# Performance work log

Measured on AMD Instinct MI355X. Metric: run time of the kernel, lower is better.

## Reference

```python
import jax, jax.numpy as jnp
import numpy as np

N_HEAD = 32
N_KV = 8
D = 2048
HD = D // N_HEAD
FF = 8192
EPS = 1e-5
THETA = 10000.0


def rms_norm(x, g):
    return g * x / jnp.sqrt(jnp.mean(x * x, axis=-1, keepdims=True) + EPS)


def rope(x):
    # x: [B, H, T, hd]; lucidrains interleaved RoPE
    T = x.shape[2]
    inv_freq = 1.0 / (THETA ** (jnp.arange(0, HD, 2, dtype=jnp.float32) / HD))  # [hd/2]
    freqs = jnp.arange(T, dtype=jnp.float32)[:, None] * inv_freq[None, :]       # [T, hd/2]
    freqs = jnp.repeat(freqs, 2, axis=-1)                                        # [T, hd]
    cos, sin = jnp.cos(freqs), jnp.sin(freqs)
    x1 = x[..., ::2]
    x2 = x[..., 1::2]
    rot = jnp.stack([-x2, x1], axis=-1).reshape(x.shape)
    return x * cos + rot * sin


def attention(x, wq, wk, wv, wo):
    B, T, C = x.shape
    q = (x @ wq).reshape(B, T, N_HEAD, HD).transpose(0, 2, 1, 3)  # [B,H,T,hd]
    k = (x @ wk).reshape(B, T, N_KV, HD).transpose(0, 2, 1, 3)    # [B,Hkv,T,hd]
    v = (x @ wv).reshape(B, T, N_KV, HD).transpose(0, 2, 1, 3)
    q = rope(q)
    k = rope(k)
    rep = N_HEAD // N_KV
    k = jnp.repeat(k, rep, axis=1)
    v = jnp.repeat(v, rep, axis=1)
    att = jnp.einsum('bhqd,bhkd->bhqk', q, k) * (1.0 / np.sqrt(HD))
    causal = jnp.tril(jnp.ones((T, T), dtype=bool))
    att = jnp.where(causal[None, None], att, -jnp.inf)
    att = jax.nn.softmax(att, axis=-1)
    y = jnp.einsum('bhqk,bhkd->bhqd', att, v)
    y = y.transpose(0, 2, 1, 3).reshape(B, T, C)
    return y @ wo


def mlp(x, wg, wu, wd):
    return (jax.nn.silu(x @ wg) * (x @ wu)) @ wd


def setup_inputs() -> dict:
    key = jax.random.key(0)
    ks = jax.random.split(key, 9)
    s = lambda fan_in: 1.0 / np.sqrt(fan_in)
    return {
        'x': jax.random.normal(ks[0], (1, 2048, D), dtype=jnp.float32),
        'g1': jnp.ones((D,), dtype=jnp.float32),
        'wq': jax.random.normal(ks[1], (D, D), dtype=jnp.float32) * s(D),
        'wk': jax.random.normal(ks[2], (D, N_KV * HD), dtype=jnp.float32) * s(D),
        'wv': jax.random.normal(ks[3], (D, N_KV * HD), dtype=jnp.float32) * s(D),
        'wo': jax.random.normal(ks[4], (D, D), dtype=jnp.float32) * s(D),
        'g2': jnp.ones((D,), dtype=jnp.float32),
        'wg': jax.random.normal(ks[5], (D, FF), dtype=jnp.float32) * s(D),
        'wu': jax.random.normal(ks[6], (D, FF), dtype=jnp.float32) * s(D),
        'wd': jax.random.normal(ks[7], (FF, D), dtype=jnp.float32) * s(FF),
    }


def reference(x, g1, wq, wk, wv, wo, g2, wg, wu, wd):
    residual = x
    x = rms_norm(x, g1)
    x = x + attention(x, wq, wk, wv, wo)
    x = rms_norm(x, g2)
    x = x + mlp(x, wg, wu, wd)
    x = x + residual
    return x
```

## Files before the change

### kernel.cpp

```cpp
#include <hip/hip_runtime.h>
#include <cstdint>
#include <cstddef>


typedef __attribute__((ext_vector_type(8))) short short8;
typedef __attribute__((ext_vector_type(4))) float f32x4;

typedef __attribute__((address_space(1))) const void gvoid_t;
typedef __attribute__((address_space(3))) void lvoid_t;

__device__ inline unsigned short f2b(float f) {
  unsigned int u = __float_as_uint(f);
  u += 0x7fffu + ((u >> 16) & 1u);
  return (unsigned short)(u >> 16);
}
__device__ inline float b2f(unsigned short s) {
  return __uint_as_float((unsigned int)s << 16);
}

__global__ __launch_bounds__(256) void transpose_cast(
    const float* __restrict__ W, unsigned short* __restrict__ Wt,
    int R, int ldW) {
  __shared__ unsigned short s[32 * 36];
  const int r0 = blockIdx.y * 32, c0 = blockIdx.x * 32;
  const int tr = threadIdx.x >> 3, tc = (threadIdx.x & 7) << 2;
  const float4 v = *(const float4*)(W + (size_t)(r0 + tr) * ldW + c0 + tc);
  s[tr * 36 + tc + 0] = f2b(v.x);
  s[tr * 36 + tc + 1] = f2b(v.y);
  s[tr * 36 + tc + 2] = f2b(v.z);
  s[tr * 36 + tc + 3] = f2b(v.w);
  __syncthreads();
  ushort4 o;
  o.x = s[(tc + 0) * 36 + tr];
  o.y = s[(tc + 1) * 36 + tr];
  o.z = s[(tc + 2) * 36 + tr];
  o.w = s[(tc + 3) * 36 + tr];
  *(ushort4*)(Wt + (size_t)(c0 + tr) * R + r0 + tc) = o;
}

__global__ __launch_bounds__(256) void rmsnorm(
    const float* __restrict__ X, const float* __restrict__ g,
    unsigned short* __restrict__ ob) {
  const int row = blockIdx.x;
  const float* x = X + (size_t)row * 2048;
  float ss = 0.f;
  for (int i = threadIdx.x; i < 2048; i += 256) { float v = x[i]; ss += v * v; }
  for (int off = 32; off; off >>= 1) ss += __shfl_down(ss, off, 64);
  __shared__ float red[4];
  if ((threadIdx.x & 63) == 0) red[threadIdx.x >> 6] = ss;
  __syncthreads();
  const float tot = red[0] + red[1] + red[2] + red[3];
  const float r = rsqrtf(tot * (1.f / 2048.f) + 1e-5f);
  for (int i = threadIdx.x; i < 2048; i += 256)
    ob[(size_t)row * 2048 + i] = f2b(x[i] * g[i] * r);
}

__global__ __launch_bounds__(256) void add_res(
    const unsigned short* __restrict__ h2, const float* __restrict__ x,
    float* __restrict__ out) {
  const int i = blockIdx.x * 256 + threadIdx.x;
  const ushort4 h = ((const ushort4*)h2)[i];
  const float4 xv = ((const float4*)x)[i];
  float4 o;
  o.x = xv.x + b2f(h.x); o.y = xv.y + b2f(h.y);
  o.z = xv.z + b2f(h.z); o.w = xv.w + b2f(h.w);
  ((float4*)out)[i] = o;
}

__global__ __launch_bounds__(256, 2) void gemm_bt(
    const unsigned short* __restrict__ A, const unsigned short* __restrict__ Bt,
    float* Cf, unsigned short* Cb,
    const unsigned short* add1b, const float* add2,
    int N, int Kfull, int Kchunk, int epi, int Tld,
    unsigned short* Cb2, unsigned short* Cb3) {
  __shared__ unsigned short As[128 * 64];
  __shared__ unsigned short Bs[128 * 64];
  const int tid = threadIdx.x;
  const int wave = tid >> 6, lane = tid & 63;
  const int quad = lane >> 4, l16 = lane & 15;
  const int m0 = blockIdx.y * 128, n0 = blockIdx.x * 128;
  const int wr = (wave >> 1) * 64, wc = (wave & 1) * 64;
  const int Ks = blockIdx.z * Kchunk, Ke = Ks + Kchunk;

  f32x4 acc[4][4] = {};

  for (int k0 = Ks; k0 < Ke; k0 += 64) {
#pragma unroll
    for (int p = 0; p < 4; ++p) {
      const int idx = p * 256 + tid;
      const int row = idx >> 3;
      const int kc = ((idx & 7) ^ (row & 7)) * 8;
      const unsigned short* gA = A + (size_t)(m0 + row) * Kfull + k0 + kc;
      const unsigned short* gB = Bt + (size_t)(n0 + row) * Kfull + k0 + kc;
      unsigned short* lA = As + (size_t)(p * 256 + wave * 64) * 8;
      unsigned short* lB = Bs + (size_t)(p * 256 + wave * 64) * 8;
      __builtin_amdgcn_global_load_lds((gvoid_t*)gA, (lvoid_t*)lA, 16, 0, 0);
      __builtin_amdgcn_global_load_lds((gvoid_t*)gB, (lvoid_t*)lB, 16, 0, 0);
    }
    __syncthreads();

#pragma unroll
    for (int ks = 0; ks < 2; ++ks) {
      short8 af[4], bf[4];
#pragma unroll
      for (int i = 0; i < 4; ++i) {
        const int row = wr + i * 16 + l16;
        af[i] = *(const short8*)(As + row * 64 +
                                 (((ks << 2) | quad) ^ (row & 7)) * 8);
      }
#pragma unroll
      for (int j = 0; j < 4; ++j) {
        const int row = wc + j * 16 + l16;
        bf[j] = *(const short8*)(Bs + row * 64 +
                                 (((ks << 2) | quad) ^ (row & 7)) * 8);
      }
#pragma unroll
      for (int i = 0; i < 4; ++i)
#pragma unroll
        for (int j = 0; j < 4; ++j)
          acc[i][j] = __builtin_amdgcn_mfma_f32_16x16x32_bf16(
              af[i], bf[j], acc[i][j], 0, 0, 0);
    }
    __syncthreads();
  }

  if (epi == 7 && n0 >= 2560) {
#pragma unroll
    for (int i = 0; i < 4; ++i)
#pragma unroll
      for (int j = 0; j < 4; ++j) {
        const int row = m0 + wr + i * 16 + quad * 4;
        const int col = n0 + wc + j * 16 + l16 - 2560;
        ushort4 o;
        o.x = f2b(acc[i][j][0]); o.y = f2b(acc[i][j][1]);
        o.z = f2b(acc[i][j][2]); o.w = f2b(acc[i][j][3]);
        *(ushort4*)(Cb3 + (size_t)col * Tld + row) = o;
      }
    return;
  }

#pragma unroll
  for (int i = 0; i < 4; ++i)
#pragma unroll
    for (int j = 0; j < 4; ++j) {
      const int rowb = m0 + wr + i * 16 + quad * 4;
      const int col = n0 + wc + j * 16 + l16;
      float invf = 0.f, sgn = 0.f;
      if (epi == 7) {
        const int ip = (col & 63) >> 1;
        invf = __expf(-(float)ip * 0.28782313662f);
        sgn = (col & 1) ? 1.f : -1.f;
      }
#pragma unroll
      for (int r = 0; r < 4; ++r) {
        const size_t idx = (size_t)(rowb + r) * N + col;
        const float v = acc[i][j][r];
        const float p = __shfl_xor(v, 1, 64);
        if (epi == 1) {
          Cf[idx] = v + b2f(add1b[idx]);
        } else if (epi == 3) {
          const float gt = b2f(add1b[idx]);
          Cb[idx] = f2b(gt / (1.f + __expf(-gt)) * v);
        } else if (epi == 4) {
          Cb[idx] = f2b(v);
        } else if (epi == 8) {
          atomicAdd(&Cf[idx], v);
        } else {
          float sn, cs;
          __sincosf((float)(rowb + r) * invf, &sn, &cs);
          const unsigned short o = f2b(v * cs + sgn * p * sn);
          if (col < 2048)
            Cb[(size_t)(rowb + r) * 2048 + col] = o;
          else
            Cb2[(size_t)(rowb + r) * 512 + col - 2048] = o;
        }
      }
    }
}

#define PSTR 136
__global__ __launch_bounds__(256) void flash_attn(
    const unsigned short* __restrict__ Qb, const unsigned short* __restrict__ Kb,
    const unsigned short* __restrict__ Vt, unsigned short* __restrict__ Y,
    int T) {
  __shared__ char shmem[4 * 4352];

  const int tid = threadIdx.x;
  const int wave = tid >> 6, lane = tid & 63;
  const int quad = lane >> 4, l16 = lane & 15;
  const int h = blockIdx.y;
  const int qt = gridDim.x - 1 - blockIdx.x;
  const int kvh = h >> 2;
  const int qbase = qt * 16;

  short8 aQ[2];
#pragma unroll
  for (int c = 0; c < 2; ++c)
    aQ[c] = *(const short8*)(Qb + (size_t)(qbase + l16) * 2048 + h * 64 +
                             c * 32 + quad * 8);

  float m_i[4], l_i[4];
  f32x4 Oacc[4] = {};
#pragma unroll
  for (int r = 0; r < 4; ++r) { m_i[r] = -1e30f; l_i[r] = 0.f; }

  unsigned short* Pw = (unsigned short*)(shmem + wave * 4352);
  const int nchunk = (qbase + 16 + 127) >> 7;

  for (int jt = wave; jt < nchunk; jt += 4) {
    const int k0 = jt << 7;
    f32x4 S[8];
#pragma unroll
    for (int s = 0; s < 8; ++s) {
      const size_t kr = (size_t)(k0 + s * 16 + l16) * 512 + kvh * 64;
      const short8 b0 = *(const short8*)(Kb + kr + quad * 8);
      const short8 b1 = *(const short8*)(Kb + kr + 32 + quad * 8);
      f32x4 z = {};
      z = __builtin_amdgcn_mfma_f32_16x16x32_bf16(aQ[0], b0, z, 0, 0, 0);
      z = __builtin_amdgcn_mfma_f32_16x16x32_bf16(aQ[1], b1, z, 0, 0, 0);
      S[s] = z;
    }
    float tmax[4];
#pragma unroll
    for (int r = 0; r < 4; ++r) {
      const int qrow = qbase + quad * 4 + r;
      float mx = -3e38f;
#pragma unroll
      for (int s = 0; s < 8; ++s) {
        const int key = k0 + s * 16 + l16;
        float v = S[s][r] * 0.125f;
        if (key > qrow) v = -3e38f;
        S[s][r] = v;
        mx = fmaxf(mx, v);
      }
      tmax[r] = mx;
    }
#pragma unroll
    for (int off = 1; off < 16; off <<= 1)
#pragma unroll
      for (int r = 0; r < 4; ++r)
        tmax[r] = fmaxf(tmax[r], __shfl_xor(tmax[r], off, 64));

    float alpha[4], rsum[4];
#pragma unroll
    for (int r = 0; r < 4; ++r) {
      const float mn = fmaxf(m_i[r], tmax[r]);
      alpha[r] = __expf(m_i[r] - mn);
      m_i[r] = mn;
      float acc = 0.f;
#pragma unroll
      for (int s = 0; s < 8; ++s) {
        const float p = __expf(S[s][r] - mn);
        S[s][r] = p;
        acc += p;
      }
      rsum[r] = acc;
    }
#pragma unroll
    for (int off = 1; off < 16; off <<= 1)
#pragma unroll
      for (int r = 0; r < 4; ++r)
        rsum[r] += __shfl_xor(rsum[r], off, 64);
#pragma unroll
    for (int r = 0; r < 4; ++r) l_i[r] = l_i[r] * alpha[r] + rsum[r];

#pragma unroll
    for (int s = 0; s < 8; ++s)
#pragma unroll
      for (int r = 0; r < 4; ++r)
        Pw[(quad * 4 + r) * PSTR + s * 16 + l16] = f2b(S[s][r]);
    __threadfence_block();
    short8 aP[4];
#pragma unroll
    for (int kc = 0; kc < 4; ++kc)
      aP[kc] = *(const short8*)(Pw + l16 * PSTR + kc * 32 + quad * 8);

#pragma unroll
    for (int c = 0; c < 4; ++c)
#pragma unroll
      for (int r = 0; r < 4; ++r) Oacc[c][r] *= alpha[r];
#pragma unroll
    for (int c = 0; c < 4; ++c) {
      const size_t vr = (size_t)(kvh * 64 + c * 16 + l16) * T + k0;
#pragma unroll
      for (int kc = 0; kc < 4; ++kc) {
        const short8 bV = *(const short8*)(Vt + vr + kc * 32 + quad * 8);
        Oacc[c] = __builtin_amdgcn_mfma_f32_16x16x32_bf16(aP[kc], bV,
                                                          Oacc[c], 0, 0, 0);
      }
    }
  }

  float* OWw = (float*)(shmem + wave * 4352);
  float* mw  = (float*)(shmem + wave * 4352 + 4096);
  float* lw  = (float*)(shmem + wave * 4352 + 4160);
#pragma unroll
  for (int c = 0; c < 4; ++c)
#pragma unroll
    for (int r = 0; r < 4; ++r)
      OWw[c * 256 + (quad * 4 + r) * 16 + l16] = Oacc[c][r];
  if (l16 == 0)
#pragma unroll
    for (int r = 0; r < 4; ++r) {
      mw[quad * 4 + r] = m_i[r];
      lw[quad * 4 + r] = l_i[r];
    }
  __syncthreads();

  const int c = wave;
#pragma unroll
  for (int r = 0; r < 4; ++r) {
    const int row = quad * 4 + r;
    float M = -3e38f;
#pragma unroll
    for (int w2 = 0; w2 < 4; ++w2)
      M = fmaxf(M, ((const float*)(shmem + w2 * 4352 + 4096))[row]);
    float num = 0.f, den = 0.f;
#pragma unroll
    for (int w2 = 0; w2 < 4; ++w2) {
      const float mv = ((const float*)(shmem + w2 * 4352 + 4096))[row];
      const float lv = ((const float*)(shmem + w2 * 4352 + 4160))[row];
      const float sc = __expf(mv - M);
      den += lv * sc;
      num += ((const float*)(shmem + w2 * 4352))[c * 256 + row * 16 + l16] * sc;
    }
    Y[(size_t)(qbase + row) * 2048 + h * 64 + c * 16 + l16] = f2b(num / den);
  }
}

extern "C" void kernel_launch(void* const* d_in, const int* in_sizes, int n_in,
                              void* d_out, int out_size, void* d_ws,
                              size_t ws_size, hipStream_t stream) {
  const float* x  = (const float*)d_in[0];
  const float* g1 = (const float*)d_in[1];
  const float* wq = (const float*)d_in[2];
  const float* wk = (const float*)d_in[3];
  const float* wv = (const float*)d_in[4];
  const float* wo = (const float*)d_in[5];
  const float* g2 = (const float*)d_in[6];
  const float* wg = (const float*)d_in[7];
  const float* wu = (const float*)d_in[8];
  const float* wd = (const float*)d_in[9];
  float* out = (float*)d_out;

  const int T = 2048, Dm = 2048, FF = 8192;
  char* ws = (char*)d_ws;
  const size_t MB = (size_t)1 << 20;

  unsigned short* wq_t = (unsigned short*)(ws + 0 * MB);
  unsigned short* wk_t = (unsigned short*)(ws + 8 * MB);
  unsigned short* wv_t = (unsigned short*)(ws + 10 * MB);
  unsigned short* wo_t = (unsigned short*)(ws + 12 * MB);
  unsigned short* wg_t = (unsigned short*)(ws + 20 * MB);
  unsigned short* wu_t = (unsigned short*)(ws + 52 * MB);
  unsigned short* h1_b = (unsigned short*)(ws + 84 * MB);
  unsigned short* h2_b = (unsigned short*)(ws + 92 * MB);
  float*          x2_f = (float*)(ws + 100 * MB);
  unsigned short* gate = (unsigned short*)(ws + 100 * MB);
  unsigned short* q_b  = (unsigned short*)(ws + 132 * MB);
  unsigned short* k_b  = (unsigned short*)(ws + 140 * MB);
  unsigned short* vt_b = (unsigned short*)(ws + 142 * MB);
  unsigned short* y_b  = (unsigned short*)(ws + 144 * MB);
  unsigned short* wd_t = (unsigned short*)(ws + 132 * MB);

  transpose_cast<<<dim3(64, 64), 256, 0, stream>>>(wq, wq_t, Dm, Dm);
  transpose_cast<<<dim3(16, 64), 256, 0, stream>>>(wk, wk_t, Dm, 512);
  transpose_cast<<<dim3(16, 64), 256, 0, stream>>>(wv, wv_t, Dm, 512);
  transpose_cast<<<dim3(64, 64), 256, 0, stream>>>(wo, wo_t, Dm, Dm);
  transpose_cast<<<dim3(256, 64), 256, 0, stream>>>(wg, wg_t, Dm, FF);
  transpose_cast<<<dim3(256, 64), 256, 0, stream>>>(wu, wu_t, Dm, FF);

  rmsnorm<<<T, 256, 0, stream>>>(x, g1, h1_b);

  gemm_bt<<<dim3(24, 16), 256, 0, stream>>>(h1_b, wq_t, nullptr, q_b, nullptr,
                                            nullptr, 3072, Dm, Dm, 7, T, k_b,
                                            vt_b);

  flash_attn<<<dim3(T / 16, 32), 256, 0, stream>>>(q_b, k_b, vt_b, y_b, T);

  gemm_bt<<<dim3(16, 16), 256, 0, stream>>>(y_b, wo_t, x2_f, nullptr, h1_b,
                                            nullptr, Dm, Dm, Dm, 1, 0, nullptr,
                                            nullptr);

  transpose_cast<<<dim3(64, 256), 256, 0, stream>>>(wd, wd_t, FF, Dm);

  rmsnorm<<<T, 256, 0, stream>>>(x2_f, g2, h2_b);

  gemm_bt<<<dim3(64, 16), 256, 0, stream>>>(h2_b, wg_t, nullptr, gate, nullptr,
                                            nullptr, FF, Dm, Dm, 4, 0, nullptr,
                                            nullptr);
  gemm_bt<<<dim3(64, 16), 256, 0, stream>>>(h2_b, wu_t, nullptr, gate, gate,
                                            nullptr, FF, Dm, Dm, 3, 0, nullptr,
                                            nullptr);

  add_res<<<(T * Dm / 4) / 256, 256, 0, stream>>>(h2_b, x, out);
  gemm_bt<<<dim3(16, 16, 4), 256, 0, stream>>>(gate, wd_t, out, nullptr,
                                               nullptr, nullptr, Dm, FF,
                                               FF / 4, 8, 0, nullptr, nullptr);
}
```

Before: 827.5 us.

## Rewrite flash attention with 32x32 MFMA, per-wave query tiles, register-resident P

```diff
diff --git a/kernel.cpp b/kernel.cpp
--- a/kernel.cpp
+++ b/kernel.cpp
@@ -5,6 +5,7 @@
 
 typedef __attribute__((ext_vector_type(8))) short short8;
 typedef __attribute__((ext_vector_type(4))) float f32x4;
+typedef __attribute__((ext_vector_type(16))) float f32x16;
 
 typedef __attribute__((address_space(1))) const void gvoid_t;
 typedef __attribute__((address_space(3))) void lvoid_t;
@@ -16,6 +17,11 @@
 }
 __device__ inline float b2f(unsigned short s) {
   return __uint_as_float((unsigned int)s << 16);
+}
+__device__ inline unsigned int pkbf(float lo, float hi) {
+  unsigned int r;
+  asm("v_cvt_pk_bf16_f32 %0, %1, %2" : "=v"(r) : "v"(lo), "v"(hi));
+  return r;
 }
 
 __global__ __launch_bounds__(256) void transpose_cast(
@@ -178,153 +184,127 @@
     }
 }
 
-#define PSTR 136
 __global__ __launch_bounds__(256) void flash_attn(
     const unsigned short* __restrict__ Qb, const unsigned short* __restrict__ Kb,
     const unsigned short* __restrict__ Vt, unsigned short* __restrict__ Y,
     int T) {
-  __shared__ char shmem[4 * 4352];
-
   const int tid = threadIdx.x;
   const int wave = tid >> 6, lane = tid & 63;
-  const int quad = lane >> 4, l16 = lane & 15;
-  const int h = blockIdx.y;
-  const int qt = gridDim.x - 1 - blockIdx.x;
-  const int kvh = h >> 2;
-  const int qbase = qt * 16;
-
-  short8 aQ[2];
-#pragma unroll
-  for (int c = 0; c < 2; ++c)
-    aQ[c] = *(const short8*)(Qb + (size_t)(qbase + l16) * 2048 + h * 64 +
-                             c * 32 + quad * 8);
-
-  float m_i[4], l_i[4];
-  f32x4 Oacc[4] = {};
-#pragma unroll
-  for (int r = 0; r < 4; ++r) { m_i[r] = -1e30f; l_i[r] = 0.f; }
-
-  unsigned short* Pw = (unsigned short*)(shmem + wave * 4352);
-  const int nchunk = (qbase + 16 + 127) >> 7;
-
-  for (int jt = wave; jt < nchunk; jt += 4) {
-    const int k0 = jt << 7;
-    f32x4 S[8];
-#pragma unroll
-    for (int s = 0; s < 8; ++s) {
-      const size_t kr = (size_t)(k0 + s * 16 + l16) * 512 + kvh * 64;
-      const short8 b0 = *(const short8*)(Kb + kr + quad * 8);
-      const short8 b1 = *(const short8*)(Kb + kr + 32 + quad * 8);
-      f32x4 z = {};
-      z = __builtin_amdgcn_mfma_f32_16x16x32_bf16(aQ[0], b0, z, 0, 0, 0);
-      z = __builtin_amdgcn_mfma_f32_16x16x32_bf16(aQ[1], b1, z, 0, 0, 0);
-      S[s] = z;
-    }
-    float tmax[4];
-#pragma unroll
-    for (int r = 0; r < 4; ++r) {
-      const int qrow = qbase + quad * 4 + r;
-      float mx = -3e38f;
-#pragma unroll
-      for (int s = 0; s < 8; ++s) {
-        const int key = k0 + s * 16 + l16;
-        float v = S[s][r] * 0.125f;
-        if (key > qrow) v = -3e38f;
-        S[s][r] = v;
-        mx = fmaxf(mx, v);
-      }
-      tmax[r] = mx;
-    }
-#pragma unroll
-    for (int off = 1; off < 16; off <<= 1)
-#pragma unroll
-      for (int r = 0; r < 4; ++r)
-        tmax[r] = fmaxf(tmax[r], __shfl_xor(tmax[r], off, 64));
-
-    float alpha[4], rsum[4];
-#pragma unroll
-    for (int r = 0; r < 4; ++r) {
-      const float mn = fmaxf(m_i[r], tmax[r]);
-      alpha[r] = __expf(m_i[r] - mn);
-      m_i[r] = mn;
-      float acc = 0.f;
-#pragma unroll
-      for (int s = 0; s < 8; ++s) {
-        const float p = __expf(S[s][r] - mn);
-        S[s][r] = p;
-        acc += p;
-      }
-      rsum[r] = acc;
-    }
-#pragma unroll
-    for (int off = 1; off < 16; off <<= 1)
-#pragma unroll
-      for (int r = 0; r < 4; ++r)
-        rsum[r] += __shfl_xor(rsum[r], off, 64);
-#pragma unroll
-    for (int r = 0; r < 4; ++r) l_i[r] = l_i[r] * alpha[r] + rsum[r];
-
-#pragma unroll
-    for (int s = 0; s < 8; ++s)
-#pragma unroll
-      for (int r = 0; r < 4; ++r)
-        Pw[(quad * 4 + r) * PSTR + s * 16 + l16] = f2b(S[s][r]);
-    __threadfence_block();
-    short8 aP[4];
-#pragma unroll
-    for (int kc = 0; kc < 4; ++kc)
-      aP[kc] = *(const short8*)(Pw + l16 * PSTR + kc * 32 + quad * 8);
-
-#pragma unroll
-    for (int c = 0; c < 4; ++c)
-#pragma unroll
-      for (int r = 0; r < 4; ++r) Oacc[c][r] *= alpha[r];
-#pragma unroll
-    for (int c = 0; c < 4; ++c) {
-      const size_t vr = (size_t)(kvh * 64 + c * 16 + l16) * T + k0;
-#pragma unroll
-      for (int kc = 0; kc < 4; ++kc) {
-        const short8 bV = *(const short8*)(Vt + vr + kc * 32 + quad * 8);
-        Oacc[c] = __builtin_amdgcn_mfma_f32_16x16x32_bf16(aP[kc], bV,
-                                                          Oacc[c], 0, 0, 0);
-      }
-    }
-  }
-
-  float* OWw = (float*)(shmem + wave * 4352);
-  float* mw  = (float*)(shmem + wave * 4352 + 4096);
-  float* lw  = (float*)(shmem + wave * 4352 + 4160);
-#pragma unroll
-  for (int c = 0; c < 4; ++c)
-#pragma unroll
-    for (int r = 0; r < 4; ++r)
-      OWw[c * 256 + (quad * 4 + r) * 16 + l16] = Oacc[c][r];
-  if (l16 == 0)
-#pragma unroll
-    for (int r = 0; r < 4; ++r) {
-      mw[quad * 4 + r] = m_i[r];
-      lw[quad * 4 + r] = l_i[r];
-    }
-  __syncthreads();
-
-  const int c = wave;
-#pragma unroll
-  for (int r = 0; r < 4; ++r) {
-    const int row = quad * 4 + r;
-    float M = -3e38f;
-#pragma unroll
-    for (int w2 = 0; w2 < 4; ++w2)
-      M = fmaxf(M, ((const float*)(shmem + w2 * 4352 + 4096))[row]);
-    float num = 0.f, den = 0.f;
-#pragma unroll
-    for (int w2 = 0; w2 < 4; ++w2) {
-      const float mv = ((const float*)(shmem + w2 * 4352 + 4096))[row];
-      const float lv = ((const float*)(shmem + w2 * 4352 + 4160))[row];
-      const float sc = __expf(mv - M);
-      den += lv * sc;
-      num += ((const float*)(shmem + w2 * 4352))[c * 256 + row * 16 + l16] * sc;
-    }
-    Y[(size_t)(qbase + row) * 2048 + h * 64 + c * 16 + l16] = f2b(num / den);
+  const int l32 = lane & 31, hi = lane >> 5;
+  const int h = blockIdx.y, kvh = h >> 2;
+  const int qt = (blockIdx.x + wave * 16) << 5;
+  const int qrow = qt + l32;
+
+  short8 qf[4];
+#pragma unroll
+  for (int ds = 0; ds < 4; ++ds) {
+    short8 v = *(const short8*)(Qb + (size_t)qrow * 2048 + h * 64 +
+                                ds * 16 + hi * 8);
+#pragma unroll
+    for (int e = 0; e < 8; ++e)
+      v[e] = (short)f2b(b2f((unsigned short)v[e]) * 0.125f);
+    qf[ds] = v;
+  }
+
+  const unsigned short* Kp = Kb + (size_t)l32 * 512 + kvh * 64 + hi * 8;
+  const unsigned short* Vp = Vt + (size_t)(kvh * 64 + l32) * T + hi * 8;
+
+  const int niter = (qt >> 5) + 1;
+  float m_i = -3e38f, l_i = 0.f;
+  f32x16 o0 = {}, o1 = {};
+
+  short8 kf[4], kfn[4];
+#pragma unroll
+  for (int ds = 0; ds < 4; ++ds) kf[ds] = *(const short8*)(Kp + ds * 16);
+
+  for (int it = 0; it < niter; ++it) {
+    const int k0 = it << 5;
+    short8 vf[2][2];
+#pragma unroll
+    for (int dt = 0; dt < 2; ++dt)
+#pragma unroll
+      for (int ks = 0; ks < 2; ++ks)
+        vf[dt][ks] =
+            *(const short8*)(Vp + (size_t)dt * 32 * T + k0 + ks * 16);
+    const int kn = (k0 + 32 < 2016) ? k0 + 32 : 2016;
+#pragma unroll
+    for (int ds = 0; ds < 4; ++ds)
+      kfn[ds] = *(const short8*)(Kp + (size_t)kn * 512 + ds * 16);
+
+    f32x16 S = {};
+#pragma unroll
+    for (int ds = 0; ds < 4; ++ds)
+      S = __builtin_amdgcn_mfma_f32_32x32x16_bf16(kf[ds], qf[ds], S, 0, 0, 0);
+
+    float s[16];
+#pragma unroll
+    for (int r = 0; r < 16; ++r) s[r] = S[r];
+    if (k0 == qt) {
+#pragma unroll
+      for (int r = 0; r < 16; ++r)
+        if (((r & 3) + 8 * (r >> 2) + 4 * hi) > l32) s[r] = -3e38f;
+    }
+
+    float tmax = s[0];
+#pragma unroll
+    for (int r = 1; r < 16; ++r) tmax = fmaxf(tmax, s[r]);
+    tmax = fmaxf(tmax, __shfl_xor(tmax, 32, 64));
+
+    if (!__all(tmax <= m_i + 8.f)) {
+      const float mn = fmaxf(m_i, tmax);
+      const float al = __expf(m_i - mn);
+#pragma unroll
+      for (int r = 0; r < 16; ++r) { o0[r] *= al; o1[r] *= al; }
+      l_i *= al;
+      m_i = mn;
+    }
+
+    float p[16], rs = 0.f;
+#pragma unroll
+    for (int r = 0; r < 16; ++r) { p[r] = __expf(s[r] - m_i); rs += p[r]; }
+    rs += __shfl_xor(rs, 32, 64);
+    l_i += rs;
+
+    short8 pf[2];
+#pragma unroll
+    for (int ks = 0; ks < 2; ++ks) {
+      const int rb = ks * 8;
+      const unsigned int a0 = pkbf(p[rb + 0], p[rb + 1]);
+      const unsigned int a1 = pkbf(p[rb + 2], p[rb + 3]);
+      const unsigned int b0 = pkbf(p[rb + 4], p[rb + 5]);
+      const unsigned int b1 = pkbf(p[rb + 6], p[rb + 7]);
+      const unsigned int t0 = __shfl_xor((int)(hi ? a0 : b0), 32, 64);
+      const unsigned int t1 = __shfl_xor((int)(hi ? a1 : b1), 32, 64);
+      union { unsigned int u[4]; short8 v; } pu;
+      pu.u[0] = hi ? t0 : a0;
+      pu.u[1] = hi ? t1 : a1;
+      pu.u[2] = hi ? b0 : t0;
+      pu.u[3] = hi ? b1 : t1;
+      pf[ks] = pu.v;
+    }
+
+#pragma unroll
+    for (int ks = 0; ks < 2; ++ks) {
+      o0 = __builtin_amdgcn_mfma_f32_32x32x16_bf16(vf[0][ks], pf[ks], o0,
+                                                   0, 0, 0);
+      o1 = __builtin_amdgcn_mfma_f32_32x32x16_bf16(vf[1][ks], pf[ks], o1,
+                                                   0, 0, 0);
+    }
+#pragma unroll
+    for (int ds = 0; ds < 4; ++ds) kf[ds] = kfn[ds];
+  }
+
+  const float inv = 1.f / l_i;
+  unsigned short* Yp = Y + (size_t)qrow * 2048 + h * 64 + hi * 4;
+#pragma unroll
+  for (int g = 0; g < 4; ++g) {
+    ushort4 u0, u1;
+    u0.x = f2b(o0[g * 4 + 0] * inv); u0.y = f2b(o0[g * 4 + 1] * inv);
+    u0.z = f2b(o0[g * 4 + 2] * inv); u0.w = f2b(o0[g * 4 + 3] * inv);
+    *(ushort4*)(Yp + g * 8) = u0;
+    u1.x = f2b(o1[g * 4 + 0] * inv); u1.y = f2b(o1[g * 4 + 1] * inv);
+    u1.z = f2b(o1[g * 4 + 2] * inv); u1.w = f2b(o1[g * 4 + 3] * inv);
+    *(ushort4*)(Yp + 32 + g * 8) = u1;
   }
 }
 
@@ -376,7 +356,7 @@
                                             nullptr, 3072, Dm, Dm, 7, T, k_b,
                                             vt_b);
 
-  flash_attn<<<dim3(T / 16, 32), 256, 0, stream>>>(q_b, k_b, vt_b, y_b, T);
+  flash_attn<<<dim3(16, 32), 256, 0, stream>>>(q_b, k_b, vt_b, y_b, T);
 
   gemm_bt<<<dim3(16, 16), 256, 0, stream>>>(y_b, wo_t, x2_f, nullptr, h1_b,
                                             nullptr, Dm, Dm, Dm, 1, 0, nullptr,
```

After: 721.4 us. -12.8%, faster.
